# Optimization experiments

Hardware: AMD Instinct MI355X
Metric: run time of the kernel (lower is better)

## Reference

```python
import jax, jax.numpy as jnp
import numpy as np

N_NODES = 50000
N_EDGES = 640000
IN_DIM = 4
EMBED = 128
OUT_DIM = 1
N_LAYERS = 3


def setup_inputs() -> dict:
    key = jax.random.key(0)
    ks = jax.random.split(key, 12)
    node_feats = jax.random.normal(ks[0], (N_NODES, IN_DIM), dtype=jnp.float32)
    src = jax.random.randint(ks[1], (N_EDGES,), 0, N_NODES, dtype=jnp.int64 if jax.config.x64_enabled else jnp.int32)
    dst = jax.random.randint(ks[2], (N_EDGES,), 0, N_NODES, dtype=jnp.int64 if jax.config.x64_enabled else jnp.int32)
    s = 1.0 / np.sqrt(EMBED)
    W_emb = jax.random.normal(ks[3], (IN_DIM, EMBED), dtype=jnp.float32) * (1.0 / np.sqrt(IN_DIM))
    b_emb = jnp.zeros((EMBED,), dtype=jnp.float32)
    W_g = jax.random.normal(ks[4], (N_LAYERS, EMBED, EMBED), dtype=jnp.float32) * s
    b_g = jnp.zeros((N_LAYERS, EMBED), dtype=jnp.float32)
    W_o1 = jax.random.normal(ks[5], (EMBED, EMBED), dtype=jnp.float32) * s
    b_o1 = jnp.zeros((EMBED,), dtype=jnp.float32)
    W_o2 = jax.random.normal(ks[6], (EMBED, OUT_DIM), dtype=jnp.float32) * s
    b_o2 = jnp.zeros((OUT_DIM,), dtype=jnp.float32)
    return {"node_feats": node_feats, "src": src, "dst": dst,
            "W_emb": W_emb, "b_emb": b_emb, "W_g": W_g, "b_g": b_g,
            "W_o1": W_o1, "b_o1": b_o1, "W_o2": W_o2, "b_o2": b_o2}


def reference(node_feats, src, dst, W_emb, b_emb, W_g, b_g, W_o1, b_o1, W_o2, b_o2):
    n = node_feats.shape[0]
    ones = jnp.ones(src.shape[0], dtype=node_feats.dtype)
    # DGL GraphConv norm='both': symmetric degree normalization, degrees clamped to >=1
    out_deg = jnp.clip(jax.ops.segment_sum(ones, src, num_segments=n), 1.0)
    in_deg = jnp.clip(jax.ops.segment_sum(ones, dst, num_segments=n), 1.0)
    norm_src = (out_deg ** -0.5)[:, None]  # [N,1]
    norm_dst = (in_deg ** -0.5)[:, None]   # [N,1]

    h = node_feats @ W_emb + b_emb  # [N, E]
    for l in range(W_g.shape[0]):
        x = h * norm_src                                        # scale sources
        agg = jax.ops.segment_sum(x[src], dst, num_segments=n)  # SpMM gather/scatter
        h = agg * norm_dst
        h = h @ W_g[l] + b_g[l]
        h = jax.nn.relu(h)
    h = jax.nn.relu(h @ W_o1 + b_o1)
    return h @ W_o2 + b_o2  # [N, out_dim]
```

## Files before the change

### kernel.cpp

```cpp
#include <hip/hip_runtime.h>

#define NN 50000
#define NE 640000
#define NPAD 50176
#define SCAN_B 196
#define OUT_CHUNKS 64
#define OUT_CE 10000
#define IN_CHUNKS 128
#define IN_CE 5000

typedef short bf16x8 __attribute__((ext_vector_type(8)));
typedef float f32x4 __attribute__((ext_vector_type(4)));

__device__ __forceinline__ unsigned short f2bf(float f) {
  unsigned int u = __float_as_uint(f);
  unsigned int r = (u + 0x7FFFu + ((u >> 16) & 1u)) >> 16;
  return (unsigned short)r;
}
__device__ __forceinline__ float bf2f(unsigned short h) {
  return __uint_as_float(((unsigned int)h) << 16);
}

typedef const __attribute__((address_space(1))) void* gptr_t;
typedef __attribute__((address_space(3))) void* lptr_t;
__device__ __forceinline__ void gload16(const void* g, void* l) {
  __builtin_amdgcn_global_load_lds((gptr_t)g, (lptr_t)l, 16, 0, 0);
}

__global__ __launch_bounds__(256) void k_hist(const int* __restrict__ src,
                                              const int* __restrict__ dst,
                                              unsigned short* __restrict__ hist_out,
                                              unsigned short* __restrict__ hist_in) {
  __shared__ unsigned int h[NPAD / 2];
  int b = blockIdx.x, tid = threadIdx.x;
  for (int i = tid; i < NPAD / 2; i += 256) h[i] = 0;
  __syncthreads();
  if (b < OUT_CHUNKS) {
    int base = b * OUT_CE;
    for (int i = tid; i < OUT_CE; i += 256) {
      int n = src[base + i];
      atomicAdd(&h[n >> 1], (n & 1) ? 0x10000u : 1u);
    }
  } else {
    int base = (b - OUT_CHUNKS) * IN_CE;
    for (int i = tid; i < IN_CE; i += 256) {
      int n = dst[base + i];
      atomicAdd(&h[n >> 1], (n & 1) ? 0x10000u : 1u);
    }
  }
  __syncthreads();
  unsigned int* outp = (unsigned int*)((b < OUT_CHUNKS ? hist_out : hist_in) +
                                       (size_t)(b < OUT_CHUNKS ? b : b - OUT_CHUNKS) * NPAD);
  for (int i = tid; i < NPAD / 2; i += 256) outp[i] = h[i];
}

__global__ __launch_bounds__(256) void k_scan1(const unsigned short* __restrict__ hist_out,
                                               unsigned short* __restrict__ hist_in,
                                               float* __restrict__ nsrc,
                                               float* __restrict__ ndst,
                                               int* __restrict__ in_cnt,
                                               int* __restrict__ bsum) {
  int t = threadIdx.x, n = blockIdx.x * 256 + t;
  int tot_in = 0;
  if (n < NN) {
    int od = 0;
#pragma unroll 8
    for (int c = 0; c < OUT_CHUNKS; ++c) od += hist_out[(size_t)c * NPAD + n];
    int pf = 0;
#pragma unroll 8
    for (int c = 0; c < IN_CHUNKS; ++c) {
      size_t idx = (size_t)c * NPAD + n;
      unsigned short v = hist_in[idx];
      hist_in[idx] = (unsigned short)pf;
      pf += v;
    }
    tot_in = pf;
    in_cnt[n] = tot_in;
    nsrc[n] = 1.0f / sqrtf((float)max(od, 1));
    ndst[n] = 1.0f / sqrtf((float)max(tot_in, 1));
  }
  int s = tot_in;
#pragma unroll
  for (int o = 32; o >= 1; o >>= 1) s += __shfl_down(s, o);
  __shared__ int ws4[4];
  if ((t & 63) == 0) ws4[t >> 6] = s;
  __syncthreads();
  if (t == 0) bsum[blockIdx.x] = ws4[0] + ws4[1] + ws4[2] + ws4[3];
}

__global__ __launch_bounds__(256) void k_scan3(const int* __restrict__ in_cnt,
                                               const int* __restrict__ bsum,
                                               int* __restrict__ row_start) {
  int b = blockIdx.x, t = threadIdx.x, lane = t & 63, w = t >> 6;
  __shared__ int wtot[4];
  __shared__ int sbase;
  {
    int v = (t < b) ? bsum[t] : 0;
#pragma unroll
    for (int o = 32; o >= 1; o >>= 1) v += __shfl_down(v, o);
    if (lane == 0) wtot[w] = v;
    __syncthreads();
    if (t == 0) sbase = wtot[0] + wtot[1] + wtot[2] + wtot[3];
    __syncthreads();
  }
  int i = b * 256 + t;
  int v = (i < NN) ? in_cnt[i] : 0;
  int sc = v;
#pragma unroll
  for (int o = 1; o < 64; o <<= 1) {
    int x = __shfl_up(sc, o);
    if (lane >= o) sc += x;
  }
  if (lane == 63) wtot[w] = sc;
  __syncthreads();
  int base = sbase;
  for (int j = 0; j < w; ++j) base += wtot[j];
  if (i < NN) row_start[i] = base + sc - v;
}

__global__ __launch_bounds__(256) void k_fill(const int* __restrict__ src,
                                              const int* __restrict__ dst,
                                              const int* __restrict__ row_start,
                                              const unsigned short* __restrict__ prefix,
                                              int* __restrict__ col) {
  __shared__ unsigned int h[NPAD / 2];
  int c = blockIdx.x, tid = threadIdx.x;
  for (int i = tid; i < NPAD / 2; i += 256) h[i] = 0;
  __syncthreads();
  int base = c * IN_CE;
  for (int i = tid; i < IN_CE; i += 256) {
    int d = dst[base + i];
    unsigned int old = atomicAdd(&h[d >> 1], (d & 1) ? 0x10000u : 1u);
    int rank = (d & 1) ? (int)(old >> 16) : (int)(old & 0xFFFFu);
    col[row_start[d] + (int)prefix[(size_t)c * NPAD + d] + rank] = src[base + i];
  }
}

__global__ __launch_bounds__(256) void k_embed_prep(const float* __restrict__ nf,
                                                    const float* __restrict__ W,
                                                    const float* __restrict__ b,
                                                    const float* __restrict__ nsrc,
                                                    float* __restrict__ xs,
                                                    const float* __restrict__ Wg,
                                                    const float* __restrict__ Wo1,
                                                    unsigned short* __restrict__ wt) {
  int bid = blockIdx.x;
  if (bid < 25000) {
    int idx = bid * 256 + threadIdx.x;
    int n = idx >> 7, j = idx & 127;
    const float* f = nf + n * 4;
    float acc = b[j];
    acc += f[0] * W[j] + f[1] * W[128 + j] + f[2] * W[256 + j] + f[3] * W[384 + j];
    xs[idx] = acc * nsrc[n];
  } else {
    int idx = (bid - 25000) * 256 + threadIdx.x;
    int mat = idx >> 14, rem = idx & 16383;
    int k = rem >> 7, n = rem & 127;
    const float* Wsrc = (mat < 3) ? (Wg + mat * 16384) : Wo1;
    float v = Wsrc[k * 128 + n];
    unsigned short hi = f2bf(v);
    float lo = v - bf2f(hi);
    unsigned short* basep = wt + mat * 32768;
    basep[n * 128 + k] = hi;
    basep[16384 + n * 128 + k] = f2bf(lo);
  }
}

__global__ __launch_bounds__(256) void k_spmm(const float* __restrict__ xs,
                                              unsigned short* __restrict__ ahi,
                                              unsigned short* __restrict__ alo,
                                              const int* __restrict__ col,
                                              const int* __restrict__ row_start,
                                              const int* __restrict__ in_cnt,
                                              const float* __restrict__ ndst) {
  int node = blockIdx.x * 4 + (threadIdx.x >> 6);
  int lane = threadIdx.x & 63;
  int half = lane >> 5;
  int ql = lane & 31;
  int start = row_start[node];
  int cnt = in_cnt[node];
  float4 acc = make_float4(0.f, 0.f, 0.f, 0.f);
  const float4* X4 = (const float4*)xs;
  for (int base = 0; base < cnt; base += 64) {
    int m = min(cnt - base, 64);
    int ccol = (lane < m) ? col[start + base + lane] : 0;
    for (int jj = 0; jj < m; jj += 8) {
      int i0 = jj + half, i1 = i0 + 2, i2 = i0 + 4, i3 = i0 + 6;
      int mm = m - 1;
      int s0 = __shfl(ccol, min(i0, mm));
      int s1 = __shfl(ccol, min(i1, mm));
      int s2 = __shfl(ccol, min(i2, mm));
      int s3 = __shfl(ccol, min(i3, mm));
      float f0 = (i0 < m) ? 1.f : 0.f;
      float f1 = (i1 < m) ? 1.f : 0.f;
      float f2 = (i2 < m) ? 1.f : 0.f;
      float f3 = (i3 < m) ? 1.f : 0.f;
      float4 v0 = X4[(size_t)s0 * 32 + ql];
      float4 v1 = X4[(size_t)s1 * 32 + ql];
      float4 v2 = X4[(size_t)s2 * 32 + ql];
      float4 v3 = X4[(size_t)s3 * 32 + ql];
      acc.x = fmaf(f0, v0.x, acc.x); acc.y = fmaf(f0, v0.y, acc.y);
      acc.z = fmaf(f0, v0.z, acc.z); acc.w = fmaf(f0, v0.w, acc.w);
      acc.x = fmaf(f1, v1.x, acc.x); acc.y = fmaf(f1, v1.y, acc.y);
      acc.z = fmaf(f1, v1.z, acc.z); acc.w = fmaf(f1, v1.w, acc.w);
      acc.x = fmaf(f2, v2.x, acc.x); acc.y = fmaf(f2, v2.y, acc.y);
      acc.z = fmaf(f2, v2.z, acc.z); acc.w = fmaf(f2, v2.w, acc.w);
      acc.x = fmaf(f3, v3.x, acc.x); acc.y = fmaf(f3, v3.y, acc.y);
      acc.z = fmaf(f3, v3.z, acc.z); acc.w = fmaf(f3, v3.w, acc.w);
    }
  }
  acc.x += __shfl_down(acc.x, 32);
  acc.y += __shfl_down(acc.y, 32);
  acc.z += __shfl_down(acc.z, 32);
  acc.w += __shfl_down(acc.w, 32);
  if (half == 0) {
    float nd = ndst[node];
    float v0 = acc.x * nd, v1 = acc.y * nd, v2 = acc.z * nd, v3 = acc.w * nd;
    ushort4 h, l;
    h.x = f2bf(v0); l.x = f2bf(v0 - bf2f(h.x));
    h.y = f2bf(v1); l.y = f2bf(v1 - bf2f(h.y));
    h.z = f2bf(v2); l.z = f2bf(v2 - bf2f(h.z));
    h.w = f2bf(v3); l.w = f2bf(v3 - bf2f(h.w));
    *(ushort4*)(ahi + (size_t)node * 128 + ql * 4) = h;
    *(ushort4*)(alo + (size_t)node * 128 + ql * 4) = l;
  }
}

__global__ __launch_bounds__(256) void k_gemm_mfma(
    const unsigned short* __restrict__ Ahi, const unsigned short* __restrict__ Alo,
    const unsigned short* __restrict__ Wth, const unsigned short* __restrict__ Wtl,
    const float* __restrict__ bias, float* __restrict__ outf,
    unsigned short* __restrict__ outhi, unsigned short* __restrict__ outlo,
    const float* __restrict__ nsrc, const float* __restrict__ W_o2,
    const float* __restrict__ b_o2, int M, int mode) {
  __shared__ unsigned short sm[2 * 64 * 128];
  __shared__ float smred[4][64];
  int tid = threadIdx.x;
  int lane = tid & 63, w = tid >> 6;
  int tile0 = blockIdx.x * 64;

  {
    int slot = lane & 15;
#pragma unroll
    for (int j = 0; j < 4; ++j) {
      int ldsoff = w * 4096 + j * 1024;
      int row = (ldsoff >> 8) + (lane >> 4);
      int grow = tile0 + row;
      if (grow > M - 1) grow = M - 1;
      size_t gsrc = (size_t)grow * 256 + (size_t)(((slot ^ (row & 7)) << 4));
      gload16((const char*)Ahi + gsrc, (char*)sm + ldsoff);
      gload16((const char*)Alo + gsrc, (char*)sm + 16384 + ldsoff);
    }
  }

  bf16x8 bh[2][4], bl[2][4];
  {
    int koff = (lane >> 4) * 8;
#pragma unroll
    for (int cf = 0; cf < 2; ++cf) {
      int n = w * 32 + cf * 16 + (lane & 15);
      const unsigned short* ph = Wth + (size_t)n * 128 + koff;
      const unsigned short* pl = Wtl + (size_t)n * 128 + koff;
#pragma unroll
      for (int kc = 0; kc < 4; ++kc) {
        bh[cf][kc] = *(const bf16x8*)(ph + kc * 32);
        bl[cf][kc] = *(const bf16x8*)(pl + kc * 32);
      }
    }
  }

  f32x4 acc[4][2] = {};
  __syncthreads();

  int r15 = lane & 15, kq = lane >> 4;
  for (int kc = 0; kc < 4; ++kc) {
    bf16x8 ah[4], al[4];
#pragma unroll
    for (int m = 0; m < 4; ++m) {
      int row = m * 16 + r15;
      int boff = row * 256 + ((((kc * 4 + kq) ^ (row & 7))) << 4);
      ah[m] = *(const bf16x8*)((const char*)sm + boff);
      al[m] = *(const bf16x8*)((const char*)sm + 16384 + boff);
    }
#pragma unroll
    for (int m = 0; m < 4; ++m)
#pragma unroll
      for (int cf = 0; cf < 2; ++cf) {
        acc[m][cf] = __builtin_amdgcn_mfma_f32_16x16x32_bf16(ah[m], bh[cf][kc], acc[m][cf], 0, 0, 0);
        acc[m][cf] = __builtin_amdgcn_mfma_f32_16x16x32_bf16(ah[m], bl[cf][kc], acc[m][cf], 0, 0, 0);
        acc[m][cf] = __builtin_amdgcn_mfma_f32_16x16x32_bf16(al[m], bh[cf][kc], acc[m][cf], 0, 0, 0);
      }
  }

  if (mode == 3) {
    float w2v[2], bv2[2];
#pragma unroll
    for (int cf = 0; cf < 2; ++cf) {
      int colg = w * 32 + cf * 16 + r15;
      w2v[cf] = W_o2[colg];
      bv2[cf] = bias[colg];
    }
#pragma unroll
    for (int m = 0; m < 4; ++m) {
#pragma unroll
      for (int i = 0; i < 4; ++i) {
        float p = fmaxf(acc[m][0][i] + bv2[0], 0.f) * w2v[0] +
                  fmaxf(acc[m][1][i] + bv2[1], 0.f) * w2v[1];
#pragma unroll
        for (int msk = 1; msk < 16; msk <<= 1) p += __shfl_xor(p, msk);
        if (r15 == 0) smred[w][m * 16 + kq * 4 + i] = p;
      }
    }
    __syncthreads();
    if (tid < 64) {
      int gr = tile0 + tid;
      if (gr < M)
        outf[gr] = smred[0][tid] + smred[1][tid] + smred[2][tid] + smred[3][tid] + b_o2[0];
    }
    return;
  }
#pragma unroll
  for (int cf = 0; cf < 2; ++cf) {
    int colg = w * 32 + cf * 16 + r15;
    float bv = bias[colg];
#pragma unroll
    for (int m = 0; m < 4; ++m) {
#pragma unroll
      for (int i = 0; i < 4; ++i) {
        int gr = tile0 + m * 16 + kq * 4 + i;
        if (gr < M) {
          float v = fmaxf(acc[m][cf][i] + bv, 0.f);
          if (mode == 0) {
            outf[(size_t)gr * 128 + colg] = v * nsrc[gr];
          } else {
            unsigned short h = f2bf(v);
            outhi[(size_t)gr * 128 + colg] = h;
            outlo[(size_t)gr * 128 + colg] = f2bf(v - bf2f(h));
          }
        }
      }
    }
  }
}

extern "C" void kernel_launch(void* const* d_in, const int* in_sizes, int n_in,
                              void* d_out, int out_size, void* d_ws, size_t ws_size,
                              hipStream_t stream) {
  const float* node_feats = (const float*)d_in[0];
  const int* src = (const int*)d_in[1];
  const int* dst = (const int*)d_in[2];
  const float* W_emb = (const float*)d_in[3];
  const float* b_emb = (const float*)d_in[4];
  const float* W_g = (const float*)d_in[5];
  const float* b_g = (const float*)d_in[6];
  const float* W_o1 = (const float*)d_in[7];
  const float* b_o1 = (const float*)d_in[8];
  const float* W_o2 = (const float*)d_in[9];
  const float* b_o2 = (const float*)d_in[10];
  float* out = (float*)d_out;

  char* ws = (char*)d_ws;
  int* in_cnt    = (int*)(ws + 0);
  int* row_start = (int*)(ws + 200704);
  float* nsrc    = (float*)(ws + 401408);
  float* ndst    = (float*)(ws + 602112);
  int* bsum      = (int*)(ws + 802816);
  int* col       = (int*)(ws + 803840);
  unsigned short* wt = (unsigned short*)(ws + 3363840);
  float* X       = (float*)(ws + 3625984);
  unsigned short* Xu = (unsigned short*)(ws + 3625984);
  unsigned short* hist_out = (unsigned short*)(ws + 3625984);
  unsigned short* hist_in  = (unsigned short*)(ws + 3625984 + 6422528);
  unsigned short* Ahi = (unsigned short*)(ws + 29225984);
  unsigned short* Alo = (unsigned short*)(ws + 42025984);

  k_hist<<<OUT_CHUNKS + IN_CHUNKS, 256, 0, stream>>>(src, dst, hist_out, hist_in);
  k_scan1<<<SCAN_B, 256, 0, stream>>>(hist_out, hist_in, nsrc, ndst, in_cnt, bsum);
  k_scan3<<<SCAN_B, 256, 0, stream>>>(in_cnt, bsum, row_start);
  k_fill<<<IN_CHUNKS, 256, 0, stream>>>(src, dst, row_start, hist_in, col);
  k_embed_prep<<<25256, 256, 0, stream>>>(node_feats, W_emb, b_emb, nsrc, X,
                                          W_g, W_o1, wt);

  int gemm_grid = (NN + 63) / 64;
  for (int l = 0; l < 3; ++l) {
    k_spmm<<<NN / 4, 256, 0, stream>>>(X, Ahi, Alo, col, row_start, in_cnt, ndst);
    unsigned short* wth = wt + l * 32768;
    unsigned short* wtl = wth + 16384;
    if (l < 2) {
      k_gemm_mfma<<<gemm_grid, 256, 0, stream>>>(Ahi, Alo, wth, wtl, b_g + l * 128,
                                                 X, nullptr, nullptr, nsrc,
                                                 nullptr, nullptr, NN, 0);
    } else {
      k_gemm_mfma<<<gemm_grid, 256, 0, stream>>>(Ahi, Alo, wth, wtl, b_g + l * 128,
                                                 nullptr, Xu, Xu + 6400000, nsrc,
                                                 nullptr, nullptr, NN, 1);
    }
  }
  k_gemm_mfma<<<gemm_grid, 256, 0, stream>>>(Xu, Xu + 6400000, wt + 3 * 32768,
                                             wt + 3 * 32768 + 16384, b_o1,
                                             out, nullptr, nullptr, nsrc,
                                             W_o2, b_o2, NN, 3);
}
```

Before: 361.6 us.

## Fuse SpMM aggregation with layer GEMM and output MLP into one kernel

Each layer now runs as a single kernel. Every 64-row block first gathers and aggregates neighbor features straight into LDS in split-bf16 form, then runs the MFMA GEMM from LDS. This removes the global round-trip of the aggregated hi/lo buffers and the separate launches. The last layer also chains the W_o1 GEMM and the W_o2 reduction in the same block, using ping-pong X buffers. In exchange, each block has only 4 waves doing the sparse gather, with one grid of 782 blocks in place of 12500, so the gather may have less latency hiding and lower occupancy.

```diff
diff --git a/kernel.cpp b/kernel.cpp
--- a/kernel.cpp
+++ b/kernel.cpp
@@ -19,12 +19,6 @@
 }
 __device__ __forceinline__ float bf2f(unsigned short h) {
   return __uint_as_float(((unsigned int)h) << 16);
-}
-
-typedef const __attribute__((address_space(1))) void* gptr_t;
-typedef __attribute__((address_space(3))) void* lptr_t;
-__device__ __forceinline__ void gload16(const void* g, void* l) {
-  __builtin_amdgcn_global_load_lds((gptr_t)g, (lptr_t)l, 16, 0, 0);
 }
 
 __global__ __launch_bounds__(256) void k_hist(const int* __restrict__ src,
@@ -166,92 +160,21 @@
   }
 }
 
-__global__ __launch_bounds__(256) void k_spmm(const float* __restrict__ xs,
-                                              unsigned short* __restrict__ ahi,
-                                              unsigned short* __restrict__ alo,
-                                              const int* __restrict__ col,
-                                              const int* __restrict__ row_start,
-                                              const int* __restrict__ in_cnt,
-                                              const float* __restrict__ ndst) {
-  int node = blockIdx.x * 4 + (threadIdx.x >> 6);
-  int lane = threadIdx.x & 63;
-  int half = lane >> 5;
-  int ql = lane & 31;
-  int start = row_start[node];
-  int cnt = in_cnt[node];
-  float4 acc = make_float4(0.f, 0.f, 0.f, 0.f);
-  const float4* X4 = (const float4*)xs;
-  for (int base = 0; base < cnt; base += 64) {
-    int m = min(cnt - base, 64);
-    int ccol = (lane < m) ? col[start + base + lane] : 0;
-    for (int jj = 0; jj < m; jj += 8) {
-      int i0 = jj + half, i1 = i0 + 2, i2 = i0 + 4, i3 = i0 + 6;
-      int mm = m - 1;
-      int s0 = __shfl(ccol, min(i0, mm));
-      int s1 = __shfl(ccol, min(i1, mm));
-      int s2 = __shfl(ccol, min(i2, mm));
-      int s3 = __shfl(ccol, min(i3, mm));
-      float f0 = (i0 < m) ? 1.f : 0.f;
-      float f1 = (i1 < m) ? 1.f : 0.f;
-      float f2 = (i2 < m) ? 1.f : 0.f;
-      float f3 = (i3 < m) ? 1.f : 0.f;
-      float4 v0 = X4[(size_t)s0 * 32 + ql];
-      float4 v1 = X4[(size_t)s1 * 32 + ql];
-      float4 v2 = X4[(size_t)s2 * 32 + ql];
-      float4 v3 = X4[(size_t)s3 * 32 + ql];
-      acc.x = fmaf(f0, v0.x, acc.x); acc.y = fmaf(f0, v0.y, acc.y);
-      acc.z = fmaf(f0, v0.z, acc.z); acc.w = fmaf(f0, v0.w, acc.w);
-      acc.x = fmaf(f1, v1.x, acc.x); acc.y = fmaf(f1, v1.y, acc.y);
-      acc.z = fmaf(f1, v1.z, acc.z); acc.w = fmaf(f1, v1.w, acc.w);
-      acc.x = fmaf(f2, v2.x, acc.x); acc.y = fmaf(f2, v2.y, acc.y);
-      acc.z = fmaf(f2, v2.z, acc.z); acc.w = fmaf(f2, v2.w, acc.w);
-      acc.x = fmaf(f3, v3.x, acc.x); acc.y = fmaf(f3, v3.y, acc.y);
-      acc.z = fmaf(f3, v3.z, acc.z); acc.w = fmaf(f3, v3.w, acc.w);
-    }
-  }
-  acc.x += __shfl_down(acc.x, 32);
-  acc.y += __shfl_down(acc.y, 32);
-  acc.z += __shfl_down(acc.z, 32);
-  acc.w += __shfl_down(acc.w, 32);
-  if (half == 0) {
-    float nd = ndst[node];
-    float v0 = acc.x * nd, v1 = acc.y * nd, v2 = acc.z * nd, v3 = acc.w * nd;
-    ushort4 h, l;
-    h.x = f2bf(v0); l.x = f2bf(v0 - bf2f(h.x));
-    h.y = f2bf(v1); l.y = f2bf(v1 - bf2f(h.y));
-    h.z = f2bf(v2); l.z = f2bf(v2 - bf2f(h.z));
-    h.w = f2bf(v3); l.w = f2bf(v3 - bf2f(h.w));
-    *(ushort4*)(ahi + (size_t)node * 128 + ql * 4) = h;
-    *(ushort4*)(alo + (size_t)node * 128 + ql * 4) = l;
-  }
-}
-
-__global__ __launch_bounds__(256) void k_gemm_mfma(
-    const unsigned short* __restrict__ Ahi, const unsigned short* __restrict__ Alo,
+__global__ __launch_bounds__(256) void k_layer(
+    const float* __restrict__ xs, const int* __restrict__ col,
+    const int* __restrict__ row_start, const int* __restrict__ in_cnt,
+    const float* __restrict__ ndst, const float* __restrict__ nsrc,
     const unsigned short* __restrict__ Wth, const unsigned short* __restrict__ Wtl,
     const float* __restrict__ bias, float* __restrict__ outf,
-    unsigned short* __restrict__ outhi, unsigned short* __restrict__ outlo,
-    const float* __restrict__ nsrc, const float* __restrict__ W_o2,
+    const unsigned short* __restrict__ W2h, const unsigned short* __restrict__ W2l,
+    const float* __restrict__ bias2, const float* __restrict__ W_o2,
     const float* __restrict__ b_o2, int M, int mode) {
   __shared__ unsigned short sm[2 * 64 * 128];
   __shared__ float smred[4][64];
   int tid = threadIdx.x;
   int lane = tid & 63, w = tid >> 6;
+  int half = lane >> 5, ql = lane & 31;
   int tile0 = blockIdx.x * 64;
-
-  {
-    int slot = lane & 15;
-#pragma unroll
-    for (int j = 0; j < 4; ++j) {
-      int ldsoff = w * 4096 + j * 1024;
-      int row = (ldsoff >> 8) + (lane >> 4);
-      int grow = tile0 + row;
-      if (grow > M - 1) grow = M - 1;
-      size_t gsrc = (size_t)grow * 256 + (size_t)(((slot ^ (row & 7)) << 4));
-      gload16((const char*)Ahi + gsrc, (char*)sm + ldsoff);
-      gload16((const char*)Alo + gsrc, (char*)sm + 16384 + ldsoff);
-    }
-  }
 
   bf16x8 bh[2][4], bl[2][4];
   {
@@ -269,9 +192,57 @@
     }
   }
 
+  const float4* X4 = (const float4*)xs;
+  for (int it = 0; it < 16; ++it) {
+    int row = it * 4 + w;
+    int node = tile0 + row;
+    float4 acc = make_float4(0.f, 0.f, 0.f, 0.f);
+    int start = 0, cnt = 0;
+    if (node < M) { start = row_start[node]; cnt = in_cnt[node]; }
+    for (int base = 0; base < cnt; base += 64) {
+      int m = min(cnt - base, 64);
+      int ccol = (lane < m) ? col[start + base + lane] : 0;
+      for (int jj = 0; jj < m; jj += 16) {
+        int mm = m - 1;
+        float4 v[8];
+        float f[8];
+#pragma unroll
+        for (int u = 0; u < 8; ++u) {
+          int idx = jj + u * 2 + half;
+          int s = __shfl(ccol, min(idx, mm));
+          f[u] = (idx < m) ? 1.f : 0.f;
+          v[u] = X4[(size_t)s * 32 + ql];
+        }
+#pragma unroll
+        for (int u = 0; u < 8; ++u) {
+          acc.x = fmaf(f[u], v[u].x, acc.x);
+          acc.y = fmaf(f[u], v[u].y, acc.y);
+          acc.z = fmaf(f[u], v[u].z, acc.z);
+          acc.w = fmaf(f[u], v[u].w, acc.w);
+        }
+      }
+    }
+    acc.x += __shfl_down(acc.x, 32);
+    acc.y += __shfl_down(acc.y, 32);
+    acc.z += __shfl_down(acc.z, 32);
+    acc.w += __shfl_down(acc.w, 32);
+    if (half == 0) {
+      float nd = (node < M) ? ndst[node] : 0.f;
+      float v0 = acc.x * nd, v1 = acc.y * nd, v2 = acc.z * nd, v3 = acc.w * nd;
+      ushort4 h, l;
+      h.x = f2bf(v0); l.x = f2bf(v0 - bf2f(h.x));
+      h.y = f2bf(v1); l.y = f2bf(v1 - bf2f(h.y));
+      h.z = f2bf(v2); l.z = f2bf(v2 - bf2f(h.z));
+      h.w = f2bf(v3); l.w = f2bf(v3 - bf2f(h.w));
+      int c = ql >> 1;
+      int boff = row * 256 + ((c ^ (row & 7)) << 4) + (ql & 1) * 8;
+      *(ushort4*)((char*)sm + boff) = h;
+      *(ushort4*)((char*)sm + 16384 + boff) = l;
+    }
+  }
+  __syncthreads();
+
   f32x4 acc[4][2] = {};
-  __syncthreads();
-
   int r15 = lane & 15, kq = lane >> 4;
   for (int kc = 0; kc < 4; ++kc) {
     bf16x8 ah[4], al[4];
@@ -292,54 +263,103 @@
       }
   }
 
-  if (mode == 3) {
-    float w2v[2], bv2[2];
+  if (mode == 0) {
 #pragma unroll
     for (int cf = 0; cf < 2; ++cf) {
       int colg = w * 32 + cf * 16 + r15;
-      w2v[cf] = W_o2[colg];
-      bv2[cf] = bias[colg];
-    }
-#pragma unroll
-    for (int m = 0; m < 4; ++m) {
-#pragma unroll
-      for (int i = 0; i < 4; ++i) {
-        float p = fmaxf(acc[m][0][i] + bv2[0], 0.f) * w2v[0] +
-                  fmaxf(acc[m][1][i] + bv2[1], 0.f) * w2v[1];
-#pragma unroll
-        for (int msk = 1; msk < 16; msk <<= 1) p += __shfl_xor(p, msk);
-        if (r15 == 0) smred[w][m * 16 + kq * 4 + i] = p;
-      }
-    }
-    __syncthreads();
-    if (tid < 64) {
-      int gr = tile0 + tid;
-      if (gr < M)
-        outf[gr] = smred[0][tid] + smred[1][tid] + smred[2][tid] + smred[3][tid] + b_o2[0];
+      float bv = bias[colg];
+#pragma unroll
+      for (int m = 0; m < 4; ++m) {
+#pragma unroll
+        for (int i = 0; i < 4; ++i) {
+          int gr = tile0 + m * 16 + kq * 4 + i;
+          if (gr < M) {
+            float v = fmaxf(acc[m][cf][i] + bv, 0.f);
+            outf[(size_t)gr * 128 + colg] = v * nsrc[gr];
+          }
+        }
+      }
     }
     return;
   }
+
+  __syncthreads();
 #pragma unroll
   for (int cf = 0; cf < 2; ++cf) {
     int colg = w * 32 + cf * 16 + r15;
     float bv = bias[colg];
+    int c2 = colg >> 3, cb = (colg & 7) * 2;
 #pragma unroll
     for (int m = 0; m < 4; ++m) {
 #pragma unroll
       for (int i = 0; i < 4; ++i) {
-        int gr = tile0 + m * 16 + kq * 4 + i;
-        if (gr < M) {
-          float v = fmaxf(acc[m][cf][i] + bv, 0.f);
-          if (mode == 0) {
-            outf[(size_t)gr * 128 + colg] = v * nsrc[gr];
-          } else {
-            unsigned short h = f2bf(v);
-            outhi[(size_t)gr * 128 + colg] = h;
-            outlo[(size_t)gr * 128 + colg] = f2bf(v - bf2f(h));
-          }
-        }
-      }
-    }
+        int row = m * 16 + kq * 4 + i;
+        float v = fmaxf(acc[m][cf][i] + bv, 0.f);
+        unsigned short h = f2bf(v);
+        int boff = row * 256 + ((c2 ^ (row & 7)) << 4) + cb;
+        *(unsigned short*)((char*)sm + boff) = h;
+        *(unsigned short*)((char*)sm + 16384 + boff) = f2bf(v - bf2f(h));
+      }
+    }
+  }
+  bf16x8 b2h[2][4], b2l[2][4];
+  {
+    int koff = (lane >> 4) * 8;
+#pragma unroll
+    for (int cf = 0; cf < 2; ++cf) {
+      int n = w * 32 + cf * 16 + (lane & 15);
+      const unsigned short* ph = W2h + (size_t)n * 128 + koff;
+      const unsigned short* pl = W2l + (size_t)n * 128 + koff;
+#pragma unroll
+      for (int kc = 0; kc < 4; ++kc) {
+        b2h[cf][kc] = *(const bf16x8*)(ph + kc * 32);
+        b2l[cf][kc] = *(const bf16x8*)(pl + kc * 32);
+      }
+    }
+  }
+  f32x4 acc2[4][2] = {};
+  __syncthreads();
+  for (int kc = 0; kc < 4; ++kc) {
+    bf16x8 ah[4], al[4];
+#pragma unroll
+    for (int m = 0; m < 4; ++m) {
+      int row = m * 16 + r15;
+      int boff = row * 256 + ((((kc * 4 + kq) ^ (row & 7))) << 4);
+      ah[m] = *(const bf16x8*)((const char*)sm + boff);
+      al[m] = *(const bf16x8*)((const char*)sm + 16384 + boff);
+    }
+#pragma unroll
+    for (int m = 0; m < 4; ++m)
+#pragma unroll
+      for (int cf = 0; cf < 2; ++cf) {
+        acc2[m][cf] = __builtin_amdgcn_mfma_f32_16x16x32_bf16(ah[m], b2h[cf][kc], acc2[m][cf], 0, 0, 0);
+        acc2[m][cf] = __builtin_amdgcn_mfma_f32_16x16x32_bf16(ah[m], b2l[cf][kc], acc2[m][cf], 0, 0, 0);
+        acc2[m][cf] = __builtin_amdgcn_mfma_f32_16x16x32_bf16(al[m], b2h[cf][kc], acc2[m][cf], 0, 0, 0);
+      }
+  }
+  float w2v[2], bv2[2];
+#pragma unroll
+  for (int cf = 0; cf < 2; ++cf) {
+    int colg = w * 32 + cf * 16 + r15;
+    w2v[cf] = W_o2[colg];
+    bv2[cf] = bias2[colg];
+  }
+#pragma unroll
+  for (int m = 0; m < 4; ++m) {
+#pragma unroll
+    for (int i = 0; i < 4; ++i) {
+      float p = fmaxf(acc2[m][0][i] + bv2[0], 0.f) * w2v[0] +
+                fmaxf(acc2[m][1][i] + bv2[1], 0.f) * w2v[1];
+#pragma unroll
+      for (int msk = 1; msk < 16; msk <<= 1) p += __shfl_xor(p, msk);
+      if (r15 == 0) smred[w][m * 16 + kq * 4 + i] = p;
+    }
+  }
+  __syncthreads();
+  if (tid < 64) {
+    int gr = tile0 + tid;
+    if (gr < M)
+      outf[gr] = smred[0][tid] + smred[1][tid] + smred[2][tid] + smred[3][tid] + b_o2[0];
   }
 }
 
@@ -367,37 +387,30 @@
   int* bsum      = (int*)(ws + 802816);
   int* col       = (int*)(ws + 803840);
   unsigned short* wt = (unsigned short*)(ws + 3363840);
-  float* X       = (float*)(ws + 3625984);
-  unsigned short* Xu = (unsigned short*)(ws + 3625984);
+  float* Xa      = (float*)(ws + 3625984);
   unsigned short* hist_out = (unsigned short*)(ws + 3625984);
   unsigned short* hist_in  = (unsigned short*)(ws + 3625984 + 6422528);
-  unsigned short* Ahi = (unsigned short*)(ws + 29225984);
-  unsigned short* Alo = (unsigned short*)(ws + 42025984);
+  float* Xb      = (float*)(ws + 29225984);
 
   k_hist<<<OUT_CHUNKS + IN_CHUNKS, 256, 0, stream>>>(src, dst, hist_out, hist_in);
   k_scan1<<<SCAN_B, 256, 0, stream>>>(hist_out, hist_in, nsrc, ndst, in_cnt, bsum);
   k_scan3<<<SCAN_B, 256, 0, stream>>>(in_cnt, bsum, row_start);
   k_fill<<<IN_CHUNKS, 256, 0, stream>>>(src, dst, row_start, hist_in, col);
-  k_embed_prep<<<25256, 256, 0, stream>>>(node_feats, W_emb, b_emb, nsrc, X,
+  k_embed_prep<<<25256, 256, 0, stream>>>(node_feats, W_emb, b_emb, nsrc, Xa,
                                           W_g, W_o1, wt);
 
-  int gemm_grid = (NN + 63) / 64;
-  for (int l = 0; l < 3; ++l) {
-    k_spmm<<<NN / 4, 256, 0, stream>>>(X, Ahi, Alo, col, row_start, in_cnt, ndst);
-    unsigned short* wth = wt + l * 32768;
-    unsigned short* wtl = wth + 16384;
-    if (l < 2) {
-      k_gemm_mfma<<<gemm_grid, 256, 0, stream>>>(Ahi, Alo, wth, wtl, b_g + l * 128,
-                                                 X, nullptr, nullptr, nsrc,
-                                                 nullptr, nullptr, NN, 0);
-    } else {
-      k_gemm_mfma<<<gemm_grid, 256, 0, stream>>>(Ahi, Alo, wth, wtl, b_g + l * 128,
-                                                 nullptr, Xu, Xu + 6400000, nsrc,
-                                                 nullptr, nullptr, NN, 1);
-    }
-  }
-  k_gemm_mfma<<<gemm_grid, 256, 0, stream>>>(Xu, Xu + 6400000, wt + 3 * 32768,
-                                             wt + 3 * 32768 + 16384, b_o1,
-                                             out, nullptr, nullptr, nsrc,
-                                             W_o2, b_o2, NN, 3);
-}
+  int grid = (NN + 63) / 64;
+  k_layer<<<grid, 256, 0, stream>>>(Xa, col, row_start, in_cnt, ndst, nsrc,
+                                    wt + 0 * 32768, wt + 0 * 32768 + 16384,
+                                    b_g + 0, Xb, nullptr, nullptr, nullptr,
+                                    nullptr, nullptr, NN, 0);
+  k_layer<<<grid, 256, 0, stream>>>(Xb, col, row_start, in_cnt, ndst, nsrc,
+                                    wt + 1 * 32768, wt + 1 * 32768 + 16384,
+                                    b_g + 128, Xa, nullptr, nullptr, nullptr,
+                                    nullptr, nullptr, NN, 0);
+  k_layer<<<grid, 256, 0, stream>>>(Xa, col, row_start, in_cnt, ndst, nsrc,
+                                    wt + 2 * 32768, wt + 2 * 32768 + 16384,
+                                    b_g + 256, out,
+                                    wt + 3 * 32768, wt + 3 * 32768 + 16384,
+                                    b_o1, W_o2, b_o2, NN, 2);
+}
```

Result: slower. 387.5 us (+7.2%).

## Slice feature matrix into 16-column panels for cache-local SpMM gathers

Applied to the files above, without the earlier changes.

The node feature matrix is stored as 8 column slices of 16 floats per node, and the SpMM grid is multiplied by 8 so that each block handles one slice for 4 nodes. Each wavefront gathers 16 neighbors at once (4 lanes per 64-byte row) and reduces across lanes with xor shuffles. The aim is to give each pass a 3.2 MB working set that fits in cache better than full 512-byte rows. In exchange, the col and row_start reads are repeated 8 times, the grid is 8x larger, and the GEMM epilogue writes are strided.

```diff
diff --git a/kernel.cpp b/kernel.cpp
--- a/kernel.cpp
+++ b/kernel.cpp
@@ -140,7 +140,7 @@
                                                     const float* __restrict__ W,
                                                     const float* __restrict__ b,
                                                     const float* __restrict__ nsrc,
-                                                    float* __restrict__ xs,
+                                                    float* __restrict__ xt,
                                                     const float* __restrict__ Wg,
                                                     const float* __restrict__ Wo1,
                                                     unsigned short* __restrict__ wt) {
@@ -151,7 +151,7 @@
     const float* f = nf + n * 4;
     float acc = b[j];
     acc += f[0] * W[j] + f[1] * W[128 + j] + f[2] * W[256 + j] + f[3] * W[384 + j];
-    xs[idx] = acc * nsrc[n];
+    xt[(size_t)(j >> 4) * NN * 16 + (size_t)n * 16 + (j & 15)] = acc * nsrc[n];
   } else {
     int idx = (bid - 25000) * 256 + threadIdx.x;
     int mat = idx >> 14, rem = idx & 16383;
@@ -166,54 +166,55 @@
   }
 }
 
-__global__ __launch_bounds__(256) void k_spmm(const float* __restrict__ xs,
+__global__ __launch_bounds__(256) void k_spmm(const float* __restrict__ xt,
                                               unsigned short* __restrict__ ahi,
                                               unsigned short* __restrict__ alo,
                                               const int* __restrict__ col,
                                               const int* __restrict__ row_start,
                                               const int* __restrict__ in_cnt,
                                               const float* __restrict__ ndst) {
-  int node = blockIdx.x * 4 + (threadIdx.x >> 6);
+  int s = blockIdx.x & 7;
+  int node = (blockIdx.x >> 3) * 4 + (threadIdx.x >> 6);
   int lane = threadIdx.x & 63;
-  int half = lane >> 5;
-  int ql = lane & 31;
+  int slot = lane >> 2, sub = lane & 3;
+  const float4* Xs = (const float4*)(xt + (size_t)s * NN * 16);
   int start = row_start[node];
   int cnt = in_cnt[node];
   float4 acc = make_float4(0.f, 0.f, 0.f, 0.f);
-  const float4* X4 = (const float4*)xs;
   for (int base = 0; base < cnt; base += 64) {
     int m = min(cnt - base, 64);
     int ccol = (lane < m) ? col[start + base + lane] : 0;
-    for (int jj = 0; jj < m; jj += 8) {
-      int i0 = jj + half, i1 = i0 + 2, i2 = i0 + 4, i3 = i0 + 6;
-      int mm = m - 1;
-      int s0 = __shfl(ccol, min(i0, mm));
-      int s1 = __shfl(ccol, min(i1, mm));
-      int s2 = __shfl(ccol, min(i2, mm));
-      int s3 = __shfl(ccol, min(i3, mm));
-      float f0 = (i0 < m) ? 1.f : 0.f;
-      float f1 = (i1 < m) ? 1.f : 0.f;
-      float f2 = (i2 < m) ? 1.f : 0.f;
-      float f3 = (i3 < m) ? 1.f : 0.f;
-      float4 v0 = X4[(size_t)s0 * 32 + ql];
-      float4 v1 = X4[(size_t)s1 * 32 + ql];
-      float4 v2 = X4[(size_t)s2 * 32 + ql];
-      float4 v3 = X4[(size_t)s3 * 32 + ql];
-      acc.x = fmaf(f0, v0.x, acc.x); acc.y = fmaf(f0, v0.y, acc.y);
-      acc.z = fmaf(f0, v0.z, acc.z); acc.w = fmaf(f0, v0.w, acc.w);
-      acc.x = fmaf(f1, v1.x, acc.x); acc.y = fmaf(f1, v1.y, acc.y);
-      acc.z = fmaf(f1, v1.z, acc.z); acc.w = fmaf(f1, v1.w, acc.w);
-      acc.x = fmaf(f2, v2.x, acc.x); acc.y = fmaf(f2, v2.y, acc.y);
-      acc.z = fmaf(f2, v2.z, acc.z); acc.w = fmaf(f2, v2.w, acc.w);
-      acc.x = fmaf(f3, v3.x, acc.x); acc.y = fmaf(f3, v3.y, acc.y);
-      acc.z = fmaf(f3, v3.z, acc.z); acc.w = fmaf(f3, v3.w, acc.w);
-    }
-  }
-  acc.x += __shfl_down(acc.x, 32);
-  acc.y += __shfl_down(acc.y, 32);
-  acc.z += __shfl_down(acc.z, 32);
-  acc.w += __shfl_down(acc.w, 32);
-  if (half == 0) {
+    int mm = m - 1;
+    int i0 = slot, i1 = slot + 16, i2 = slot + 32, i3 = slot + 48;
+    int s0 = __shfl(ccol, min(i0, mm));
+    int s1 = __shfl(ccol, min(i1, mm));
+    int s2 = __shfl(ccol, min(i2, mm));
+    int s3 = __shfl(ccol, min(i3, mm));
+    float f0 = (i0 < m) ? 1.f : 0.f;
+    float f1 = (i1 < m) ? 1.f : 0.f;
+    float f2 = (i2 < m) ? 1.f : 0.f;
+    float f3 = (i3 < m) ? 1.f : 0.f;
+    float4 v0 = Xs[(size_t)s0 * 4 + sub];
+    float4 v1 = Xs[(size_t)s1 * 4 + sub];
+    float4 v2 = Xs[(size_t)s2 * 4 + sub];
+    float4 v3 = Xs[(size_t)s3 * 4 + sub];
+    acc.x = fmaf(f0, v0.x, acc.x); acc.y = fmaf(f0, v0.y, acc.y);
+    acc.z = fmaf(f0, v0.z, acc.z); acc.w = fmaf(f0, v0.w, acc.w);
+    acc.x = fmaf(f1, v1.x, acc.x); acc.y = fmaf(f1, v1.y, acc.y);
+    acc.z = fmaf(f1, v1.z, acc.z); acc.w = fmaf(f1, v1.w, acc.w);
+    acc.x = fmaf(f2, v2.x, acc.x); acc.y = fmaf(f2, v2.y, acc.y);
+    acc.z = fmaf(f2, v2.z, acc.z); acc.w = fmaf(f2, v2.w, acc.w);
+    acc.x = fmaf(f3, v3.x, acc.x); acc.y = fmaf(f3, v3.y, acc.y);
+    acc.z = fmaf(f3, v3.z, acc.z); acc.w = fmaf(f3, v3.w, acc.w);
+  }
+#pragma unroll
+  for (int o = 4; o < 64; o <<= 1) {
+    acc.x += __shfl_xor(acc.x, o);
+    acc.y += __shfl_xor(acc.y, o);
+    acc.z += __shfl_xor(acc.z, o);
+    acc.w += __shfl_xor(acc.w, o);
+  }
+  if (lane < 4) {
     float nd = ndst[node];
     float v0 = acc.x * nd, v1 = acc.y * nd, v2 = acc.z * nd, v3 = acc.w * nd;
     ushort4 h, l;
@@ -221,8 +222,9 @@
     h.y = f2bf(v1); l.y = f2bf(v1 - bf2f(h.y));
     h.z = f2bf(v2); l.z = f2bf(v2 - bf2f(h.z));
     h.w = f2bf(v3); l.w = f2bf(v3 - bf2f(h.w));
-    *(ushort4*)(ahi + (size_t)node * 128 + ql * 4) = h;
-    *(ushort4*)(alo + (size_t)node * 128 + ql * 4) = l;
+    int off = node * 128 + s * 16 + sub * 4;
+    *(ushort4*)(ahi + off) = h;
+    *(ushort4*)(alo + off) = l;
   }
 }
 
@@ -323,6 +325,7 @@
   for (int cf = 0; cf < 2; ++cf) {
     int colg = w * 32 + cf * 16 + r15;
     float bv = bias[colg];
+    int sl = colg >> 4, so = colg & 15;
 #pragma unroll
     for (int m = 0; m < 4; ++m) {
 #pragma unroll
@@ -331,7 +334,7 @@
         if (gr < M) {
           float v = fmaxf(acc[m][cf][i] + bv, 0.f);
           if (mode == 0) {
-            outf[(size_t)gr * 128 + colg] = v * nsrc[gr];
+            outf[(size_t)sl * NN * 16 + (size_t)gr * 16 + so] = v * nsrc[gr];
           } else {
             unsigned short h = f2bf(v);
             outhi[(size_t)gr * 128 + colg] = h;
@@ -382,8 +385,9 @@
                                           W_g, W_o1, wt);
 
   int gemm_grid = (NN + 63) / 64;
+  int spmm_grid = (NN / 4) * 8;
   for (int l = 0; l < 3; ++l) {
-    k_spmm<<<NN / 4, 256, 0, stream>>>(X, Ahi, Alo, col, row_start, in_cnt, ndst);
+    k_spmm<<<spmm_grid, 256, 0, stream>>>(X, Ahi, Alo, col, row_start, in_cnt, ndst);
     unsigned short* wth = wt + l * 32768;
     unsigned short* wtl = wth + 16384;
     if (l < 2) {
```

Result: slower. 608.3 us (+68.2%).
